# Kernel optimization log

Hardware: AMD Instinct MI355X
Metric: run time of the kernel (lower is better)

The kernel has to match this reference:

```python
import jax, jax.numpy as jnp
import numpy as np

N = 500000
D = 112
H = 64
W = 176


def setup_inputs() -> dict:
    key = jax.random.key(0)
    k1, k2 = jax.random.split(key)
    # positions: x in [0, W-1), y in [0, H-1)
    u = jax.random.uniform(k1, (N, 2), dtype=jnp.float32)
    sampling_positions = u * jnp.array([W - 1.0, H - 1.0], dtype=jnp.float32)
    sampling_depth_features = jax.random.normal(k2, (N, D), dtype=jnp.float32)
    return {
        "sampling_positions": sampling_positions,
        "sampling_depth_features": sampling_depth_features,
        "height": H,
        "width": W,
    }


def _bilinear_scatter(positions, features, height, width):
    # positions: [N,2] (x, y); features: [N,D] -> grid [H,W,D]
    x = positions[:, 0]
    y = positions[:, 1]
    x0 = jnp.floor(x)
    y0 = jnp.floor(y)
    wx = x - x0
    wy = y - y0
    x0i = x0.astype(jnp.int32)
    y0i = y0.astype(jnp.int32)
    x1i = x0i + 1
    y1i = y0i + 1

    out = jnp.zeros((height, width, features.shape[1]), dtype=jnp.float32)

    def in_bounds(yi, xi):
        return (yi >= 0) & (yi < height) & (xi >= 0) & (xi < width)

    corners = [
        (y0i, x0i, (1.0 - wy) * (1.0 - wx)),
        (y0i, x1i, (1.0 - wy) * wx),
        (y1i, x0i, wy * (1.0 - wx)),
        (y1i, x1i, wy * wx),
    ]
    for yi, xi, w in corners:
        valid = in_bounds(yi, xi)
        w = jnp.where(valid, w, 0.0)
        yi = jnp.clip(yi, 0, height - 1)
        xi = jnp.clip(xi, 0, width - 1)
        out = out.at[yi, xi].add(w[:, None] * features)
    return out


def reference(sampling_positions, sampling_depth_features, height, width):
    return _bilinear_scatter(sampling_positions, sampling_depth_features, height, width)
```

## Files before the change

### kernel.cpp

```cpp
#include <hip/hip_runtime.h>


#define D     112
#define D2    56
#define H     64
#define W     176
#define HW    (H * W)
#define CAP   128
#define CSTR  16
#define TY    4
#define TX    4
#define GX    (W / TX)
#define GY    (H / TY)
#define NCELL (TY * TX)
#define NW    16
#define NBIN  25
#define NSLOT (NBIN * CAP)

__device__ __forceinline__ void fill_one(int p, float x, float y,
                                         int* cnt, uint2* bucket)
{
    float xf = floorf(x), yf = floorf(y);
    float wx = x - xf,    wy = y - yf;
    int x0 = min(max((int)xf, 0), W - 1);
    int y0 = min(max((int)yf, 0), H - 1);
    int bin = y0 * W + x0;
    unsigned qw = (__float2uint_rn(wy * 65535.0f) << 16)
                |  __float2uint_rn(wx * 65535.0f);
    int i = atomicAdd(&cnt[bin * CSTR], 1);
    if (i < CAP) bucket[(size_t)bin * CAP + i] = make_uint2((unsigned)p, qw);
}

__global__ __launch_bounds__(256) void fill_kernel(
    const float2* __restrict__ pos,
    int* __restrict__ cnt,
    uint2* __restrict__ bucket,
    int N)
{
    int i = blockIdx.x * blockDim.x + threadIdx.x;
    int p0 = 4 * i;
    if (p0 >= N) return;
    const float4* p4 = (const float4*)pos;
    if (p0 + 3 < N) {
        float4 a = p4[2 * i];
        float4 b = p4[2 * i + 1];
        fill_one(p0,     a.x, a.y, cnt, bucket);
        fill_one(p0 + 1, a.z, a.w, cnt, bucket);
        fill_one(p0 + 2, b.x, b.y, cnt, bucket);
        fill_one(p0 + 3, b.z, b.w, cnt, bucket);
    } else {
        for (int k = 0; k < 4 && p0 + k < N; ++k) {
            float2 q = pos[p0 + k];
            fill_one(p0 + k, q.x, q.y, cnt, bucket);
        }
    }
}

__global__ __launch_bounds__(1024, 8) void accum_kernel(
    const float* __restrict__ feat,
    const int* __restrict__ cnt,
    const uint2* __restrict__ bucket,
    float* __restrict__ out)
{
    const int tile = blockIdx.x;
    const int ty0  = (tile / GX) * TY;
    const int tx0  = (tile % GX) * TX;
    const int t    = threadIdx.x;
    const int wid  = t >> 6;
    const int lane = t & 63;
    const bool act = lane < D2;

    __shared__ int sn[NBIN];
    __shared__ __align__(16) union {
        uint2  hdr[NSLOT];
        float2 sacc[4][NCELL][D2];
    } sm;

    if (t < NBIN) {
        int by = t / 5 - 1, bx = t % 5 - 1;
        int gby = ty0 + by, gbx = tx0 + bx;
        int n = 0;
        if (gby >= 0 && gbx >= 0 && gbx < W)
            n = min(cnt[(gby * W + gbx) * CSTR], CAP);
        sn[t] = n;
    }
    __syncthreads();

    for (int i = t; i < NSLOT; i += 1024) {
        int b = i >> 7, s = i & (CAP - 1);
        if (s < sn[b]) {
            int by = b / 5 - 1, bx = b % 5 - 1;
            int gbin = (ty0 + by) * W + (tx0 + bx);
            sm.hdr[i] = bucket[(size_t)gbin * CAP + s];
        }
    }
    __syncthreads();

    float2 acc[NCELL];
#pragma unroll
    for (int c = 0; c < NCELL; ++c) acc[c] = make_float2(0.0f, 0.0f);

#pragma unroll
    for (int by = -1; by < TY; ++by) {
#pragma unroll
        for (int bx = -1; bx < TX; ++bx) {
            const int b  = (by + 1) * 5 + (bx + 1);
            const int n  = sn[b];
            const int lo = (n * wid) >> 4;
            const int hi = (n * (wid + 1)) >> 4;
            const uint2* hb = sm.hdr + b * CAP;

            auto proc = [&](uint2 en, float2 f) {
                float wx = (float)(en.y & 0xffffu) * (1.0f / 65535.0f);
                float wy = (float)(en.y >> 16)     * (1.0f / 65535.0f);
                float ax = 1.0f - wx, ay = 1.0f - wy;
#pragma unroll
                for (int dy = 0; dy < 2; ++dy) {
                    const int cy = by + dy;
                    if (cy < 0 || cy >= TY) continue;
                    const float fy = dy ? wy : ay;
#pragma unroll
                    for (int dx = 0; dx < 2; ++dx) {
                        const int cx = bx + dx;
                        if (cx < 0 || cx >= TX) continue;
                        const float fw = fy * (dx ? wx : ax);
                        const int c = cy * TX + cx;
                        acc[c].x = fmaf(fw, f.x, acc[c].x);
                        acc[c].y = fmaf(fw, f.y, acc[c].y);
                    }
                }
            };
            auto ldrow = [&](unsigned p) -> float2 {
                return act ? ((const float2*)(feat + (size_t)p * D))[lane]
                           : make_float2(0.0f, 0.0f);
            };

            for (int e0 = lo; e0 < hi; e0 += 4) {
                const int m = hi - e0;
                uint2 h0, h1, h2, h3;
                float2 f0, f1, f2, f3;
                h0 = hb[e0];
                if (m > 1) h1 = hb[e0 + 1];
                if (m > 2) h2 = hb[e0 + 2];
                if (m > 3) h3 = hb[e0 + 3];
                f0 = ldrow(h0.x);
                if (m > 1) f1 = ldrow(h1.x);
                if (m > 2) f2 = ldrow(h2.x);
                if (m > 3) f3 = ldrow(h3.x);
                proc(h0, f0);
                if (m > 1) proc(h1, f1);
                if (m > 2) proc(h2, f2);
                if (m > 3) proc(h3, f3);
            }
        }
    }

    __syncthreads();
    const int copy = wid & 3;
    const int rnd  = wid >> 2;

    for (int w = 0; w < 4; ++w) {
        if (rnd == w && act) {
            if (w == 0) {
#pragma unroll
                for (int c = 0; c < NCELL; ++c) sm.sacc[copy][c][lane] = acc[c];
            } else {
#pragma unroll
                for (int c = 0; c < NCELL; ++c) {
                    float2 v = sm.sacc[copy][c][lane];
                    v.x += acc[c].x; v.y += acc[c].y;
                    sm.sacc[copy][c][lane] = v;
                }
            }
        }
        __syncthreads();
    }

    if (wid < NCELL && act) {
        const int c  = wid;
        const int cy = c / TX, cx = c % TX;
        float2 v0 = sm.sacc[0][c][lane];
        float2 v1 = sm.sacc[1][c][lane];
        float2 v2 = sm.sacc[2][c][lane];
        float2 v3 = sm.sacc[3][c][lane];
        float2* dst = (float2*)(out + ((size_t)(ty0 + cy) * W + (tx0 + cx)) * D);
        dst[lane] = make_float2((v0.x + v1.x) + (v2.x + v3.x),
                                (v0.y + v1.y) + (v2.y + v3.y));
    }
}

extern "C" void kernel_launch(void* const* d_in, const int* in_sizes, int n_in,
                              void* d_out, int out_size, void* d_ws, size_t ws_size,
                              hipStream_t stream) {
    const float2* pos = (const float2*)d_in[0];
    const float* feat = (const float*)d_in[1];
    float* out        = (float*)d_out;

    const int N = in_sizes[0] / 2;

    int* cnt      = (int*)d_ws;
    uint2* bucket = (uint2*)((char*)d_ws + (size_t)HW * CSTR * sizeof(int));

    hipMemsetAsync(cnt, 0, (size_t)HW * CSTR * sizeof(int), stream);

    int nq = (N + 3) / 4;
    fill_kernel<<<(nq + 255) / 256, 256, 0, stream>>>(pos, cnt, bucket, N);

    accum_kernel<<<GY * GX, 1024, 0, stream>>>(feat, cnt, bucket, out);
}
```

Before: 366.7 us.

## Fuse fill and accumulate kernels into one persistent kernel with grid barrier

Merges the bucket-fill kernel and the accumulate kernel into a single persistent launch of 256 blocks of 1024 threads. The blocks first bin a contiguous slice of points, then meet at a global atomic spin barrier, then loop over output tiles in grid-stride order. This removes one kernel launch and the gap between the two kernels. In exchange, the fill phase runs with fewer threads, the tiles may be less evenly balanced, and the barrier relies on all 256 blocks being resident at the same time.

```diff
diff --git a/kernel.cpp b/kernel.cpp
--- a/kernel.cpp
+++ b/kernel.cpp
@@ -12,10 +12,11 @@
 #define TX    4
 #define GX    (W / TX)
 #define GY    (H / TY)
+#define NT    (GY * GX)
 #define NCELL (TY * TX)
-#define NW    16
 #define NBIN  25
 #define NSLOT (NBIN * CAP)
+#define NBLK  256
 
 __device__ __forceinline__ void fill_one(int p, float x, float y,
                                          int* cnt, uint2* bucket)
@@ -31,41 +32,42 @@
     if (i < CAP) bucket[(size_t)bin * CAP + i] = make_uint2((unsigned)p, qw);
 }
 
-__global__ __launch_bounds__(256) void fill_kernel(
+__global__ __launch_bounds__(1024, 4) void fused_kernel(
     const float2* __restrict__ pos,
+    const float* __restrict__ feat,
     int* __restrict__ cnt,
     uint2* __restrict__ bucket,
-    int N)
+    float* __restrict__ out,
+    int N,
+    int* __restrict__ bar)
 {
-    int i = blockIdx.x * blockDim.x + threadIdx.x;
-    int p0 = 4 * i;
-    if (p0 >= N) return;
-    const float4* p4 = (const float4*)pos;
-    if (p0 + 3 < N) {
-        float4 a = p4[2 * i];
-        float4 b = p4[2 * i + 1];
-        fill_one(p0,     a.x, a.y, cnt, bucket);
-        fill_one(p0 + 1, a.z, a.w, cnt, bucket);
-        fill_one(p0 + 2, b.x, b.y, cnt, bucket);
-        fill_one(p0 + 3, b.z, b.w, cnt, bucket);
-    } else {
-        for (int k = 0; k < 4 && p0 + k < N; ++k) {
-            float2 q = pos[p0 + k];
-            fill_one(p0 + k, q.x, q.y, cnt, bucket);
+    const int t = threadIdx.x;
+
+    {
+        const int per  = ((N + 2 * NBLK - 1) / (2 * NBLK)) * 2;
+        const int base = blockIdx.x * per;
+        const int np   = per >> 1;
+        for (int pair = t; pair < np; pair += 1024) {
+            const int p0 = base + 2 * pair;
+            if (p0 >= N) break;
+            const float4 q = ((const float4*)pos)[(size_t)(p0 >> 1)];
+            fill_one(p0, q.x, q.y, cnt, bucket);
+            if (p0 + 1 < N) fill_one(p0 + 1, q.z, q.w, cnt, bucket);
         }
     }
-}
-
-__global__ __launch_bounds__(1024, 8) void accum_kernel(
-    const float* __restrict__ feat,
-    const int* __restrict__ cnt,
-    const uint2* __restrict__ bucket,
-    float* __restrict__ out)
-{
-    const int tile = blockIdx.x;
-    const int ty0  = (tile / GX) * TY;
-    const int tx0  = (tile % GX) * TX;
-    const int t    = threadIdx.x;
+
+    __threadfence();
+    __syncthreads();
+    if (t == 0) {
+        __hip_atomic_fetch_add(bar, 1, __ATOMIC_ACQ_REL,
+                               __HIP_MEMORY_SCOPE_AGENT);
+        while (__hip_atomic_load(bar, __ATOMIC_ACQUIRE,
+                                 __HIP_MEMORY_SCOPE_AGENT) < NBLK)
+            __builtin_amdgcn_s_sleep(2);
+    }
+    __syncthreads();
+    __threadfence();
+
     const int wid  = t >> 6;
     const int lane = t & 63;
     const bool act = lane < D2;
@@ -76,116 +78,124 @@
         float2 sacc[4][NCELL][D2];
     } sm;
 
-    if (t < NBIN) {
-        int by = t / 5 - 1, bx = t % 5 - 1;
-        int gby = ty0 + by, gbx = tx0 + bx;
-        int n = 0;
-        if (gby >= 0 && gbx >= 0 && gbx < W)
-            n = min(cnt[(gby * W + gbx) * CSTR], CAP);
-        sn[t] = n;
-    }
-    __syncthreads();
-
-    for (int i = t; i < NSLOT; i += 1024) {
-        int b = i >> 7, s = i & (CAP - 1);
-        if (s < sn[b]) {
-            int by = b / 5 - 1, bx = b % 5 - 1;
-            int gbin = (ty0 + by) * W + (tx0 + bx);
-            sm.hdr[i] = bucket[(size_t)gbin * CAP + s];
-        }
-    }
-    __syncthreads();
-
-    float2 acc[NCELL];
-#pragma unroll
-    for (int c = 0; c < NCELL; ++c) acc[c] = make_float2(0.0f, 0.0f);
-
-#pragma unroll
-    for (int by = -1; by < TY; ++by) {
-#pragma unroll
-        for (int bx = -1; bx < TX; ++bx) {
-            const int b  = (by + 1) * 5 + (bx + 1);
-            const int n  = sn[b];
-            const int lo = (n * wid) >> 4;
-            const int hi = (n * (wid + 1)) >> 4;
-            const uint2* hb = sm.hdr + b * CAP;
-
-            auto proc = [&](uint2 en, float2 f) {
-                float wx = (float)(en.y & 0xffffu) * (1.0f / 65535.0f);
-                float wy = (float)(en.y >> 16)     * (1.0f / 65535.0f);
-                float ax = 1.0f - wx, ay = 1.0f - wy;
-#pragma unroll
-                for (int dy = 0; dy < 2; ++dy) {
-                    const int cy = by + dy;
-                    if (cy < 0 || cy >= TY) continue;
-                    const float fy = dy ? wy : ay;
-#pragma unroll
-                    for (int dx = 0; dx < 2; ++dx) {
-                        const int cx = bx + dx;
-                        if (cx < 0 || cx >= TX) continue;
-                        const float fw = fy * (dx ? wx : ax);
-                        const int c = cy * TX + cx;
-                        acc[c].x = fmaf(fw, f.x, acc[c].x);
-                        acc[c].y = fmaf(fw, f.y, acc[c].y);
+    for (int tile = blockIdx.x; tile < NT; tile += NBLK) {
+        const int ty0 = (tile / GX) * TY;
+        const int tx0 = (tile % GX) * TX;
+
+        if (t < NBIN) {
+            int by = t / 5 - 1, bx = t % 5 - 1;
+            int gby = ty0 + by, gbx = tx0 + bx;
+            int n = 0;
+            if (gby >= 0 && gbx >= 0 && gbx < W)
+                n = min(cnt[(gby * W + gbx) * CSTR], CAP);
+            sn[t] = n;
+        }
+        __syncthreads();
+
+        for (int i = t; i < NSLOT; i += 1024) {
+            int b = i >> 7, s = i & (CAP - 1);
+            if (s < sn[b]) {
+                int by = b / 5 - 1, bx = b % 5 - 1;
+                int gbin = (ty0 + by) * W + (tx0 + bx);
+                sm.hdr[i] = bucket[(size_t)gbin * CAP + s];
+            }
+        }
+        __syncthreads();
+
+        float2 acc[NCELL];
+#pragma unroll
+        for (int c = 0; c < NCELL; ++c) acc[c] = make_float2(0.0f, 0.0f);
+
+#pragma unroll
+        for (int by = -1; by < TY; ++by) {
+#pragma unroll
+            for (int bx = -1; bx < TX; ++bx) {
+                const int b  = (by + 1) * 5 + (bx + 1);
+                const int n  = sn[b];
+                const int lo = (n * wid) >> 4;
+                const int hi = (n * (wid + 1)) >> 4;
+                const uint2* hb = sm.hdr + b * CAP;
+
+                auto proc = [&](uint2 en, float2 f) {
+                    float wx = (float)(en.y & 0xffffu) * (1.0f / 65535.0f);
+                    float wy = (float)(en.y >> 16)     * (1.0f / 65535.0f);
+                    float ax = 1.0f - wx, ay = 1.0f - wy;
+#pragma unroll
+                    for (int dy = 0; dy < 2; ++dy) {
+                        const int cy = by + dy;
+                        if (cy < 0 || cy >= TY) continue;
+                        const float fy = dy ? wy : ay;
+#pragma unroll
+                        for (int dx = 0; dx < 2; ++dx) {
+                            const int cx = bx + dx;
+                            if (cx < 0 || cx >= TX) continue;
+                            const float fw = fy * (dx ? wx : ax);
+                            const int c = cy * TX + cx;
+                            acc[c].x = fmaf(fw, f.x, acc[c].x);
+                            acc[c].y = fmaf(fw, f.y, acc[c].y);
+                        }
+                    }
+                };
+                auto ldrow = [&](unsigned p) -> float2 {
+                    return act ? ((const float2*)(feat + (size_t)p * D))[lane]
+                               : make_float2(0.0f, 0.0f);
+                };
+
+                for (int e0 = lo; e0 < hi; e0 += 4) {
+                    const int m = hi - e0;
+                    uint2 h0, h1, h2, h3;
+                    float2 f0, f1, f2, f3;
+                    h0 = hb[e0];
+                    if (m > 1) h1 = hb[e0 + 1];
+                    if (m > 2) h2 = hb[e0 + 2];
+                    if (m > 3) h3 = hb[e0 + 3];
+                    f0 = ldrow(h0.x);
+                    if (m > 1) f1 = ldrow(h1.x);
+                    if (m > 2) f2 = ldrow(h2.x);
+                    if (m > 3) f3 = ldrow(h3.x);
+                    proc(h0, f0);
+                    if (m > 1) proc(h1, f1);
+                    if (m > 2) proc(h2, f2);
+                    if (m > 3) proc(h3, f3);
+                }
+            }
+        }
+
+        __syncthreads();
+        const int copy = wid & 3;
+        const int rnd  = wid >> 2;
+
+        for (int w = 0; w < 4; ++w) {
+            if (rnd == w && act) {
+                if (w == 0) {
+#pragma unroll
+                    for (int c = 0; c < NCELL; ++c)
+                        sm.sacc[copy][c][lane] = acc[c];
+                } else {
+#pragma unroll
+                    for (int c = 0; c < NCELL; ++c) {
+                        float2 v = sm.sacc[copy][c][lane];
+                        v.x += acc[c].x; v.y += acc[c].y;
+                        sm.sacc[copy][c][lane] = v;
                     }
                 }
-            };
-            auto ldrow = [&](unsigned p) -> float2 {
-                return act ? ((const float2*)(feat + (size_t)p * D))[lane]
-                           : make_float2(0.0f, 0.0f);
-            };
-
-            for (int e0 = lo; e0 < hi; e0 += 4) {
-                const int m = hi - e0;
-                uint2 h0, h1, h2, h3;
-                float2 f0, f1, f2, f3;
-                h0 = hb[e0];
-                if (m > 1) h1 = hb[e0 + 1];
-                if (m > 2) h2 = hb[e0 + 2];
-                if (m > 3) h3 = hb[e0 + 3];
-                f0 = ldrow(h0.x);
-                if (m > 1) f1 = ldrow(h1.x);
-                if (m > 2) f2 = ldrow(h2.x);
-                if (m > 3) f3 = ldrow(h3.x);
-                proc(h0, f0);
-                if (m > 1) proc(h1, f1);
-                if (m > 2) proc(h2, f2);
-                if (m > 3) proc(h3, f3);
             }
-        }
-    }
-
-    __syncthreads();
-    const int copy = wid & 3;
-    const int rnd  = wid >> 2;
-
-    for (int w = 0; w < 4; ++w) {
-        if (rnd == w && act) {
-            if (w == 0) {
-#pragma unroll
-                for (int c = 0; c < NCELL; ++c) sm.sacc[copy][c][lane] = acc[c];
-            } else {
-#pragma unroll
-                for (int c = 0; c < NCELL; ++c) {
-                    float2 v = sm.sacc[copy][c][lane];
-                    v.x += acc[c].x; v.y += acc[c].y;
-                    sm.sacc[copy][c][lane] = v;
-                }
-            }
-        }
-        __syncthreads();
-    }
-
-    if (wid < NCELL && act) {
-        const int c  = wid;
-        const int cy = c / TX, cx = c % TX;
-        float2 v0 = sm.sacc[0][c][lane];
-        float2 v1 = sm.sacc[1][c][lane];
-        float2 v2 = sm.sacc[2][c][lane];
-        float2 v3 = sm.sacc[3][c][lane];
-        float2* dst = (float2*)(out + ((size_t)(ty0 + cy) * W + (tx0 + cx)) * D);
-        dst[lane] = make_float2((v0.x + v1.x) + (v2.x + v3.x),
-                                (v0.y + v1.y) + (v2.y + v3.y));
+            __syncthreads();
+        }
+
+        if (wid < NCELL && act) {
+            const int c  = wid;
+            const int cy = c / TX, cx = c % TX;
+            float2 v0 = sm.sacc[0][c][lane];
+            float2 v1 = sm.sacc[1][c][lane];
+            float2 v2 = sm.sacc[2][c][lane];
+            float2 v3 = sm.sacc[3][c][lane];
+            float2* dst =
+                (float2*)(out + ((size_t)(ty0 + cy) * W + (tx0 + cx)) * D);
+            dst[lane] = make_float2((v0.x + v1.x) + (v2.x + v3.x),
+                                    (v0.y + v1.y) + (v2.y + v3.y));
+        }
+        __syncthreads();
     }
 }
 
@@ -199,12 +209,11 @@
     const int N = in_sizes[0] / 2;
 
     int* cnt      = (int*)d_ws;
-    uint2* bucket = (uint2*)((char*)d_ws + (size_t)HW * CSTR * sizeof(int));
-
-    hipMemsetAsync(cnt, 0, (size_t)HW * CSTR * sizeof(int), stream);
-
-    int nq = (N + 3) / 4;
-    fill_kernel<<<(nq + 255) / 256, 256, 0, stream>>>(pos, cnt, bucket, N);
-
-    accum_kernel<<<GY * GX, 1024, 0, stream>>>(feat, cnt, bucket, out);
+    int* bar      = cnt + (size_t)HW * CSTR;
+    uint2* bucket = (uint2*)((char*)d_ws
+                    + ((size_t)HW * CSTR + 64) * sizeof(int));
+
+    hipMemsetAsync(cnt, 0, ((size_t)HW * CSTR + 64) * sizeof(int), stream);
+
+    fused_kernel<<<NBLK, 1024, 0, stream>>>(pos, feat, cnt, bucket, out, N, bar);
 }
```

Result: slower. 571.7 us (+55.9%).
